# Kernel tuning notes

Measured on AMD Instinct MI355X. Metric: run time of the kernel, lower is better.

The kernel has to match this reference:

```python
import jax, jax.numpy as jnp
import numpy as np

D_MODEL, N_HEADS, N_KV_HEADS = 2048, 16, 4
D_HEAD = D_MODEL // N_HEADS  # 128
N_REP = N_HEADS // N_KV_HEADS  # 4
B, S = 2, 2048
ROPE_THETA = 10000.0


def setup_inputs() -> dict:
    key = jax.random.key(0)
    ks = jax.random.split(key, 6)
    x = jax.random.normal(ks[0], (B, S, D_MODEL), dtype=jnp.float32)
    # RoPE frequencies (real/imag parts of freqs_cis)
    inv_freq = 1.0 / (ROPE_THETA ** (np.arange(0, D_HEAD, 2, dtype=np.float32) / D_HEAD))
    angles = np.arange(S, dtype=np.float32)[:, None] * inv_freq[None, :]  # [S, D_HEAD//2]
    freqs_cos = jnp.asarray(np.cos(angles))
    freqs_sin = jnp.asarray(np.sin(angles))
    # causal additive mask [1,1,S,S]
    causal = jnp.tril(jnp.ones((S, S), dtype=bool))
    mask = jnp.where(causal, 0.0, -1e9).astype(jnp.float32)[None, None]
    scale = 0.02
    wq = jax.random.normal(ks[1], (D_MODEL, N_HEADS * D_HEAD), dtype=jnp.float32) * scale
    wk = jax.random.normal(ks[2], (D_MODEL, N_KV_HEADS * D_HEAD), dtype=jnp.float32) * scale
    wv = jax.random.normal(ks[3], (D_MODEL, N_KV_HEADS * D_HEAD), dtype=jnp.float32) * scale
    wo = jax.random.normal(ks[4], (N_HEADS * D_HEAD, D_MODEL), dtype=jnp.float32) * scale
    return {"x": x, "freqs_cos": freqs_cos, "freqs_sin": freqs_sin, "mask": mask,
            "wq": wq, "wk": wk, "wv": wv, "wo": wo}


def _apply_rope(t, cos, sin):
    # t: [B, S, H, D]; cos/sin: [S, D//2] -> complex rotation on interleaved pairs
    tr = t.reshape(*t.shape[:-1], -1, 2)
    xr, xi = tr[..., 0], tr[..., 1]
    c = cos[None, :, None, :]
    s = sin[None, :, None, :]
    out_r = xr * c - xi * s
    out_i = xr * s + xi * c
    return jnp.stack([out_r, out_i], axis=-1).reshape(t.shape)


def reference(x, freqs_cos, freqs_sin, mask, wq, wk, wv, wo):
    b, s, _ = x.shape
    xq = (x @ wq).reshape(b, s, N_HEADS, D_HEAD)
    xk = (x @ wk).reshape(b, s, N_KV_HEADS, D_HEAD)
    xv = (x @ wv).reshape(b, s, N_KV_HEADS, D_HEAD)
    xq = _apply_rope(xq, freqs_cos, freqs_sin)
    xk = _apply_rope(xk, freqs_cos, freqs_sin)
    # GQA: repeat each kv head n_rep times (head h uses kv head h // n_rep)
    xk = jnp.repeat(xk, N_REP, axis=2)  # [B,S,H,D]
    xv = jnp.repeat(xv, N_REP, axis=2)
    scores = jnp.einsum("bshd,bthd->bhst", xq, xk) / jnp.sqrt(jnp.float32(D_HEAD))
    scores = scores + mask
    probs = jax.nn.softmax(scores, axis=-1)
    out = jnp.einsum("bhst,bthd->bshd", probs, xv).reshape(b, s, N_HEADS * D_HEAD)
    return out @ wo
```

## Files before the change

kernel.cpp:

```cpp
#include <hip/hip_runtime.h>
#include <hip/hip_bf16.h>

#define BB 2
#define SS 2048
#define DM 2048
#define NH 16
#define NKV 4
#define DH 128
#define QS 3072

typedef __hip_bfloat16 bf16;
typedef short short8 __attribute__((ext_vector_type(8)));
typedef float floatx4 __attribute__((ext_vector_type(4)));

#if __has_builtin(__builtin_amdgcn_exp2f)
#define EX2(x) __builtin_amdgcn_exp2f(x)
#else
#define EX2(x) exp2f(x)
#endif

__device__ __forceinline__ bf16 f2b(float v) { return __float2bfloat16(v); }
__device__ __forceinline__ short f2bs(float v) {
    bf16 t = __float2bfloat16(v);
    return __builtin_bit_cast(short, t);
}
__device__ __forceinline__ void store_c(bf16* p, float v) { *p = __float2bfloat16(v); }
__device__ __forceinline__ void store_c(float* p, float v) { *p = v; }

__global__ __launch_bounds__(256) void convert_x(const float4* __restrict__ x,
                                                 bf16* __restrict__ xb, int n4) {
    int i = blockIdx.x * blockDim.x + threadIdx.x;
    if (i >= n4) return;
    float4 v = x[i];
    bf16* p = xb + (size_t)i * 4;
    p[0] = f2b(v.x); p[1] = f2b(v.y); p[2] = f2b(v.z); p[3] = f2b(v.w);
}

__global__ __launch_bounds__(256) void convert_wT(const float* __restrict__ w,
                                                  bf16* __restrict__ outT,
                                                  int N, int Kd) {
    const int n0 = blockIdx.x * 64, k0 = blockIdx.y * 64;
    __shared__ float tile[64][65];
    const int tid = threadIdx.x;
    for (int i = tid; i < 4096; i += 256) {
        int r = i >> 6, c = i & 63;
        tile[r][c] = w[(size_t)(k0 + r) * N + n0 + c];
    }
    __syncthreads();
    for (int i = tid; i < 4096; i += 256) {
        int r = i >> 6, c = i & 63;
        outT[(size_t)(n0 + r) * Kd + k0 + c] = f2b(tile[c][r]);
    }
}

template <typename TC>
__global__ __launch_bounds__(256) void mfma_gemm(const bf16* __restrict__ A,
                                                 const bf16* __restrict__ BT,
                                                 TC* __restrict__ C,
                                                 int M, int N, int K) {
    __shared__ short As[128 * 32];
    __shared__ short Bs[128 * 32];
    const int tid = threadIdx.x;
    const int w = tid >> 6, lane = tid & 63;
    const int col16 = lane & 15, quad = lane >> 4;
    const int row0 = blockIdx.y * 128, col0 = blockIdx.x * 128;
    const int wr0 = (w >> 1) * 64, wc0 = (w & 1) * 64;

    floatx4 acc[4][4];
    #pragma unroll
    for (int mi = 0; mi < 4; mi++)
        #pragma unroll
        for (int ni = 0; ni < 4; ni++) acc[mi][ni] = (floatx4){0.f, 0.f, 0.f, 0.f};

    for (int k0 = 0; k0 < K; k0 += 32) {
        __syncthreads();
        #pragma unroll
        for (int it = 0; it < 2; it++) {
            int c = w * 128 + it * 64 + lane;
            int r = c >> 2, seg = c & 3;
            const bf16* g = A + (size_t)(row0 + r) * K + k0 + seg * 8;
            __builtin_amdgcn_global_load_lds(
                (const __attribute__((address_space(1))) unsigned int*)g,
                (__attribute__((address_space(3))) unsigned int*)&As[(w * 128 + it * 64) * 8],
                16, 0, 0);
        }
        #pragma unroll
        for (int it = 0; it < 2; it++) {
            int c = w * 128 + it * 64 + lane;
            int r = c >> 2, seg = c & 3;
            const bf16* g = BT + (size_t)(col0 + r) * K + k0 + seg * 8;
            __builtin_amdgcn_global_load_lds(
                (const __attribute__((address_space(1))) unsigned int*)g,
                (__attribute__((address_space(3))) unsigned int*)&Bs[(w * 128 + it * 64) * 8],
                16, 0, 0);
        }
        __syncthreads();

        short8 af[4], bfr[4];
        #pragma unroll
        for (int mi = 0; mi < 4; mi++)
            af[mi] = *(const short8*)&As[(wr0 + mi * 16 + col16) * 32 + quad * 8];
        #pragma unroll
        for (int ni = 0; ni < 4; ni++)
            bfr[ni] = *(const short8*)&Bs[(wc0 + ni * 16 + col16) * 32 + quad * 8];
        #pragma unroll
        for (int mi = 0; mi < 4; mi++)
            #pragma unroll
            for (int ni = 0; ni < 4; ni++)
                acc[mi][ni] = __builtin_amdgcn_mfma_f32_16x16x32_bf16(af[mi], bfr[ni], acc[mi][ni], 0, 0, 0);
    }
    #pragma unroll
    for (int mi = 0; mi < 4; mi++)
        #pragma unroll
        for (int ni = 0; ni < 4; ni++)
            #pragma unroll
            for (int r = 0; r < 4; r++)
                store_c(&C[(size_t)(row0 + wr0 + mi * 16 + quad * 4 + r) * N +
                           col0 + wc0 + ni * 16 + col16],
                        acc[mi][ni][r]);
}

__global__ void rope_kernel(bf16* __restrict__ base, const float* __restrict__ cs,
                            const float* __restrict__ sn, int n_heads, int total) {
    int idx = blockIdx.x * blockDim.x + threadIdx.x;
    if (idx >= total) return;
    int i = idx & 63;
    int h = (idx >> 6) % n_heads;
    size_t bs = (size_t)idx / (64 * n_heads);
    int s = (int)(bs % SS);
    float c = cs[s * 64 + i];
    float si = sn[s * 64 + i];
    bf16* p = base + bs * QS + h * DH + 2 * i;
    float xr = __bfloat162float(p[0]), xi = __bfloat162float(p[1]);
    p[0] = f2b(xr * c - xi * si);
    p[1] = f2b(xr * si + xi * c);
}

__global__ __launch_bounds__(256) void transpose_v(const bf16* __restrict__ qkv,
                                                   bf16* __restrict__ vt) {
    const int s0 = blockIdx.x * 64, d0 = blockIdx.y * 64;
    const int b = blockIdx.z >> 2, kvh = blockIdx.z & 3;
    __shared__ bf16 tile[64][65];
    const int tid = threadIdx.x;
    for (int i = tid; i < 4096; i += 256) {
        int r = i >> 6, c = i & 63;
        tile[r][c] = qkv[(size_t)(b * SS + s0 + r) * QS + 2560 + kvh * DH + d0 + c];
    }
    __syncthreads();
    for (int i = tid; i < 4096; i += 256) {
        int r = i >> 6, c = i & 63;
        vt[((size_t)(b * NKV + kvh) * DH + d0 + r) * SS + s0 + c] = tile[c][r];
    }
}

#define PPAD 72

__global__ __launch_bounds__(256) void flash_attn(const bf16* __restrict__ qkv,
                                                  const bf16* __restrict__ vt,
                                                  bf16* __restrict__ ao) {
    const int bx = blockIdx.x, h = blockIdx.y, b = blockIdx.z;
    const int kvh = h >> 2;
    __shared__ short Ks[2][64 * 128];
    __shared__ short Vs[2][128 * 64];
    __shared__ short Ps[4 * 16 * PPAD];
    const int tid = threadIdx.x;
    const int w = tid >> 6, lane = tid & 63;
    const int col = lane & 15, quad = lane >> 4;
    const int c7 = col & 7;
    const float C = 0.12751746517859245f;

    const int krl = lane >> 4, kseg = lane & 15;
    const int vrl = lane >> 3, vseg = lane & 7;

    const bf16* kgb = qkv + (size_t)b * SS * QS + 2048 + kvh * DH;
    const bf16* vgb = vt + (size_t)(b * NKV + kvh) * DH * SS;

    const short8 vone = {0x3F80, 0x3F80, 0x3F80, 0x3F80, 0x3F80, 0x3F80, 0x3F80, 0x3F80};

    for (int phase = 0; phase < 2; phase++) {
        const int qt = phase == 0 ? bx : (SS / 64 - 1 - bx);
        const int q0 = qt * 64;

        short8 aq[4];
        const bf16* qbase = qkv + (size_t)(b * SS + q0 + w * 16 + col) * QS + h * DH;
        #pragma unroll
        for (int kc = 0; kc < 4; kc++)
            aq[kc] = *(const short8*)(qbase + kc * 32 + quad * 8);

        floatx4 o[8];
        #pragma unroll
        for (int dt = 0; dt < 8; dt++) o[dt] = (floatx4){0.f, 0.f, 0.f, 0.f};
        floatx4 oL = (floatx4){0.f, 0.f, 0.f, 0.f};
        float mrow[4] = {-3e38f, -3e38f, -3e38f, -3e38f};

        for (int kt = 0; kt <= qt; kt++) {
            const int cur = kt & 1;
            __syncthreads();
            if (kt == 0) {
                #pragma unroll
                for (int it = 0; it < 4; it++) {
                    int row = w * 16 + it * 4 + krl;
                    const bf16* g = kgb + (size_t)row * QS + ((kseg ^ (row & 7)) * 8);
                    __builtin_amdgcn_global_load_lds(
                        (const __attribute__((address_space(1))) unsigned int*)g,
                        (__attribute__((address_space(3))) unsigned int*)&Ks[0][(w * 16 + it * 4) * 128],
                        16, 0, 0);
                }
                #pragma unroll
                for (int it = 0; it < 4; it++) {
                    int drow = w * 32 + it * 8 + vrl;
                    const bf16* g = vgb + (size_t)drow * SS + ((vseg ^ (drow & 7)) * 8);
                    __builtin_amdgcn_global_load_lds(
                        (const __attribute__((address_space(1))) unsigned int*)g,
                        (__attribute__((address_space(3))) unsigned int*)&Vs[0][(w * 32 + it * 8) * 64],
                        16, 0, 0);
                }
                __syncthreads();
            }
            if (kt < qt) {
                const int nk0 = (kt + 1) * 64;
                #pragma unroll
                for (int it = 0; it < 4; it++) {
                    int row = w * 16 + it * 4 + krl;
                    const bf16* g = kgb + (size_t)(nk0 + row) * QS + ((kseg ^ (row & 7)) * 8);
                    __builtin_amdgcn_global_load_lds(
                        (const __attribute__((address_space(1))) unsigned int*)g,
                        (__attribute__((address_space(3))) unsigned int*)&Ks[cur ^ 1][(w * 16 + it * 4) * 128],
                        16, 0, 0);
                }
                #pragma unroll
                for (int it = 0; it < 4; it++) {
                    int drow = w * 32 + it * 8 + vrl;
                    const bf16* g = vgb + (size_t)drow * SS + nk0 + ((vseg ^ (drow & 7)) * 8);
                    __builtin_amdgcn_global_load_lds(
                        (const __attribute__((address_space(1))) unsigned int*)g,
                        (__attribute__((address_space(3))) unsigned int*)&Vs[cur ^ 1][(w * 32 + it * 8) * 64],
                        16, 0, 0);
                }
            }

            const int k0 = kt * 64;
            floatx4 s[4];
            __builtin_amdgcn_s_setprio(1);
            #pragma unroll
            for (int n = 0; n < 4; n++) {
                s[n] = (floatx4){0.f, 0.f, 0.f, 0.f};
                #pragma unroll
                for (int kc = 0; kc < 4; kc++) {
                    short8 bk = *(const short8*)&Ks[cur][(n * 16 + col) * 128 + (((kc * 4 + quad) ^ c7) * 8)];
                    s[n] = __builtin_amdgcn_mfma_f32_16x16x32_bf16(aq[kc], bk, s[n], 0, 0, 0);
                }
            }
            __builtin_amdgcn_s_setprio(0);

            if (kt == qt) {
                #pragma unroll
                for (int n = 0; n < 4; n++)
                    #pragma unroll
                    for (int r = 0; r < 4; r++)
                        if ((k0 + n * 16 + col) > (q0 + w * 16 + quad * 4 + r)) s[n][r] = -3e38f;
            }

            float rmx[4];
            #pragma unroll
            for (int r = 0; r < 4; r++) {
                float rm = fmaxf(fmaxf(s[0][r], s[1][r]), fmaxf(s[2][r], s[3][r]));
                rm = fmaxf(rm, __shfl_xor(rm, 1));
                rm = fmaxf(rm, __shfl_xor(rm, 2));
                rm = fmaxf(rm, __shfl_xor(rm, 4));
                rm = fmaxf(rm, __shfl_xor(rm, 8));
                rmx[r] = fmaxf(rm, mrow[r]);
            }
            bool grow = (rmx[0] > mrow[0]) | (rmx[1] > mrow[1]) |
                        (rmx[2] > mrow[2]) | (rmx[3] > mrow[3]);
            if (__any((int)grow)) {
                float al[4];
                #pragma unroll
                for (int r = 0; r < 4; r++) {
                    al[r] = EX2((mrow[r] - rmx[r]) * C);
                    mrow[r] = rmx[r];
                }
                #pragma unroll
                for (int dt = 0; dt < 8; dt++)
                    #pragma unroll
                    for (int r = 0; r < 4; r++) o[dt][r] *= al[r];
                #pragma unroll
                for (int r = 0; r < 4; r++) oL[r] *= al[r];
            }
            float mC[4];
            #pragma unroll
            for (int r = 0; r < 4; r++) mC[r] = mrow[r] * C;

            short* pw = &Ps[w * 16 * PPAD];
            #pragma unroll
            for (int n = 0; n < 4; n++)
                #pragma unroll
                for (int r = 0; r < 4; r++)
                    pw[(quad * 4 + r) * PPAD + n * 16 + col] =
                        f2bs(EX2(__builtin_fmaf(s[n][r], C, -mC[r])));

            short8 ap0 = *(const short8*)&pw[col * PPAD + quad * 8];
            short8 ap1 = *(const short8*)&pw[col * PPAD + 32 + quad * 8];
            __builtin_amdgcn_s_setprio(1);
            #pragma unroll
            for (int dt = 0; dt < 8; dt++) {
                short8 bv0 = *(const short8*)&Vs[cur][(dt * 16 + col) * 64 + ((quad ^ c7) * 8)];
                o[dt] = __builtin_amdgcn_mfma_f32_16x16x32_bf16(ap0, bv0, o[dt], 0, 0, 0);
                short8 bv1 = *(const short8*)&Vs[cur][(dt * 16 + col) * 64 + (((quad + 4) ^ c7) * 8)];
                o[dt] = __builtin_amdgcn_mfma_f32_16x16x32_bf16(ap1, bv1, o[dt], 0, 0, 0);
            }
            oL = __builtin_amdgcn_mfma_f32_16x16x32_bf16(ap0, vone, oL, 0, 0, 0);
            oL = __builtin_amdgcn_mfma_f32_16x16x32_bf16(ap1, vone, oL, 0, 0, 0);
            __builtin_amdgcn_s_setprio(0);
        }
        #pragma unroll
        for (int r = 0; r < 4; r++) {
            float inv = 1.f / oL[r];
            int srow = q0 + w * 16 + quad * 4 + r;
            bf16* op = ao + ((size_t)(b * SS + srow) * NH + h) * DH;
            #pragma unroll
            for (int dt = 0; dt < 8; dt++)
                op[dt * 16 + col] = f2b(o[dt][r] * inv);
        }
    }
}

extern "C" void kernel_launch(void* const* d_in, const int* in_sizes, int n_in,
                              void* d_out, int out_size, void* d_ws, size_t ws_size,
                              hipStream_t stream) {
    const float* x  = (const float*)d_in[0];
    const float* fc = (const float*)d_in[1];
    const float* fs = (const float*)d_in[2];
    const float* wq = (const float*)d_in[4];
    const float* wk = (const float*)d_in[5];
    const float* wv = (const float*)d_in[6];
    const float* wo = (const float*)d_in[7];
    float* out = (float*)d_out;

    const int M = BB * SS;
    bf16* qkv    = (bf16*)d_ws;
    bf16* xb     = qkv + (size_t)M * QS;
    bf16* wqkvT  = xb + (size_t)M * DM;
    bf16* ao     = xb;
    bf16* vt     = wqkvT;
    bf16* woT    = qkv;

    dim3 blk(256);
    convert_x<<<(M * DM / 4 + 255) / 256, blk, 0, stream>>>((const float4*)x, xb, M * DM / 4);
    convert_wT<<<dim3(DM / 64, DM / 64), blk, 0, stream>>>(wq, wqkvT, DM, DM);
    convert_wT<<<dim3((NKV * DH) / 64, DM / 64), blk, 0, stream>>>(wk, wqkvT + (size_t)2048 * DM, NKV * DH, DM);
    convert_wT<<<dim3((NKV * DH) / 64, DM / 64), blk, 0, stream>>>(wv, wqkvT + (size_t)2560 * DM, NKV * DH, DM);

    mfma_gemm<bf16><<<dim3(QS / 128, M / 128), blk, 0, stream>>>(xb, wqkvT, qkv, M, QS, DM);

    const int totq = BB * SS * NH * 64;
    const int totk = BB * SS * NKV * 64;
    rope_kernel<<<(totq + 255) / 256, blk, 0, stream>>>(qkv, fc, fs, NH, totq);
    rope_kernel<<<(totk + 255) / 256, blk, 0, stream>>>(qkv + 2048, fc, fs, NKV, totk);

    transpose_v<<<dim3(SS / 64, DH / 64, BB * NKV), blk, 0, stream>>>(qkv, vt);

    flash_attn<<<dim3(SS / 128, NH, BB), blk, 0, stream>>>(qkv, vt, ao);

    convert_wT<<<dim3(DM / 64, DM / 64), blk, 0, stream>>>(wo, woT, DM, DM);
    mfma_gemm<float><<<dim3(DM / 128, M / 128), blk, 0, stream>>>(ao, woT, out, M, DM, DM);
}
```

Baseline: 366.3 us.

## Triple-buffer GEMM LDS loads with swizzle and merge weight-convert and RoPE launches

The bf16 MFMA GEMM now uses a three-stage LDS ring with async global-to-LDS loads issued two tiles ahead, so each k-step needs one barrier instead of two. An XOR swizzle on the 16-byte segments reduces LDS bank conflicts on the fragment reads, and the MFMA block is wrapped in raised wave priority. Separately, the three q/k/v weight-transpose launches are merged into one kernel and the two RoPE launches into one, which cuts launch overhead. The GEMM now uses three times as much LDS, which may lower occupancy.

```diff
diff --git a/kernel.cpp b/kernel.cpp
--- a/kernel.cpp
+++ b/kernel.cpp
@@ -53,18 +53,67 @@
     }
 }
 
+__global__ __launch_bounds__(256) void convert_wqkv(const float* __restrict__ wq,
+                                                    const float* __restrict__ wk,
+                                                    const float* __restrict__ wv,
+                                                    bf16* __restrict__ outT) {
+    const int bx = blockIdx.x;
+    const float* w; int N; int n0;
+    if (bx < 32)      { w = wq; N = 2048; n0 = bx * 64; }
+    else if (bx < 40) { w = wk; N = 512;  n0 = (bx - 32) * 64; }
+    else              { w = wv; N = 512;  n0 = (bx - 40) * 64; }
+    const int k0 = blockIdx.y * 64;
+    const int gn0 = bx * 64;
+    __shared__ float tile[64][65];
+    const int tid = threadIdx.x;
+    for (int i = tid; i < 4096; i += 256) {
+        int r = i >> 6, c = i & 63;
+        tile[r][c] = w[(size_t)(k0 + r) * N + n0 + c];
+    }
+    __syncthreads();
+    for (int i = tid; i < 4096; i += 256) {
+        int r = i >> 6, c = i & 63;
+        outT[(size_t)(gn0 + r) * DM + k0 + c] = f2b(tile[c][r]);
+    }
+}
+
 template <typename TC>
 __global__ __launch_bounds__(256) void mfma_gemm(const bf16* __restrict__ A,
                                                  const bf16* __restrict__ BT,
                                                  TC* __restrict__ C,
                                                  int M, int N, int K) {
-    __shared__ short As[128 * 32];
-    __shared__ short Bs[128 * 32];
+    __shared__ short As[3][128 * 32];
+    __shared__ short Bs[3][128 * 32];
     const int tid = threadIdx.x;
     const int w = tid >> 6, lane = tid & 63;
     const int col16 = lane & 15, quad = lane >> 4;
     const int row0 = blockIdx.y * 128, col0 = blockIdx.x * 128;
     const int wr0 = (w >> 1) * 64, wc0 = (w & 1) * 64;
+    const int nt = K / 32;
+
+    auto issue = [&](int t, int b) {
+        const int k0 = t * 32;
+        #pragma unroll
+        for (int it = 0; it < 2; it++) {
+            int cc = w * 128 + it * 64 + lane;
+            int r = cc >> 2, seg = cc & 3;
+            const bf16* g = A + (size_t)(row0 + r) * K + k0 + ((seg ^ (r & 3)) * 8);
+            __builtin_amdgcn_global_load_lds(
+                (const __attribute__((address_space(1))) unsigned int*)g,
+                (__attribute__((address_space(3))) unsigned int*)&As[b][(w * 128 + it * 64) * 8],
+                16, 0, 0);
+        }
+        #pragma unroll
+        for (int it = 0; it < 2; it++) {
+            int cc = w * 128 + it * 64 + lane;
+            int r = cc >> 2, seg = cc & 3;
+            const bf16* g = BT + (size_t)(col0 + r) * K + k0 + ((seg ^ (r & 3)) * 8);
+            __builtin_amdgcn_global_load_lds(
+                (const __attribute__((address_space(1))) unsigned int*)g,
+                (__attribute__((address_space(3))) unsigned int*)&Bs[b][(w * 128 + it * 64) * 8],
+                16, 0, 0);
+        }
+    };
 
     floatx4 acc[4][4];
     #pragma unroll
@@ -72,42 +121,36 @@
         #pragma unroll
         for (int ni = 0; ni < 4; ni++) acc[mi][ni] = (floatx4){0.f, 0.f, 0.f, 0.f};
 
-    for (int k0 = 0; k0 < K; k0 += 32) {
-        __syncthreads();
-        #pragma unroll
-        for (int it = 0; it < 2; it++) {
-            int c = w * 128 + it * 64 + lane;
-            int r = c >> 2, seg = c & 3;
-            const bf16* g = A + (size_t)(row0 + r) * K + k0 + seg * 8;
-            __builtin_amdgcn_global_load_lds(
-                (const __attribute__((address_space(1))) unsigned int*)g,
-                (__attribute__((address_space(3))) unsigned int*)&As[(w * 128 + it * 64) * 8],
-                16, 0, 0);
-        }
-        #pragma unroll
-        for (int it = 0; it < 2; it++) {
-            int c = w * 128 + it * 64 + lane;
-            int r = c >> 2, seg = c & 3;
-            const bf16* g = BT + (size_t)(col0 + r) * K + k0 + seg * 8;
-            __builtin_amdgcn_global_load_lds(
-                (const __attribute__((address_space(1))) unsigned int*)g,
-                (__attribute__((address_space(3))) unsigned int*)&Bs[(w * 128 + it * 64) * 8],
-                16, 0, 0);
-        }
-        __syncthreads();
+    issue(0, 0);
+    if (1 < nt) issue(1, 1);
+
+    for (int t = 0; t < nt; ++t) {
+        const int cb = t % 3;
+        if (t + 1 < nt) { asm volatile("s_waitcnt vmcnt(4)" ::: "memory"); }
+        else            { asm volatile("s_waitcnt vmcnt(0)" ::: "memory"); }
+        __builtin_amdgcn_sched_barrier(0);
+        __builtin_amdgcn_s_barrier();
+        __builtin_amdgcn_sched_barrier(0);
+        if (t + 2 < nt) issue(t + 2, (t + 2) % 3);
 
         short8 af[4], bfr[4];
         #pragma unroll
-        for (int mi = 0; mi < 4; mi++)
-            af[mi] = *(const short8*)&As[(wr0 + mi * 16 + col16) * 32 + quad * 8];
-        #pragma unroll
-        for (int ni = 0; ni < 4; ni++)
-            bfr[ni] = *(const short8*)&Bs[(wc0 + ni * 16 + col16) * 32 + quad * 8];
+        for (int mi = 0; mi < 4; mi++) {
+            int r = wr0 + mi * 16 + col16;
+            af[mi] = *(const short8*)&As[cb][r * 32 + ((quad ^ (r & 3)) * 8)];
+        }
+        #pragma unroll
+        for (int ni = 0; ni < 4; ni++) {
+            int r = wc0 + ni * 16 + col16;
+            bfr[ni] = *(const short8*)&Bs[cb][r * 32 + ((quad ^ (r & 3)) * 8)];
+        }
+        __builtin_amdgcn_s_setprio(1);
         #pragma unroll
         for (int mi = 0; mi < 4; mi++)
             #pragma unroll
             for (int ni = 0; ni < 4; ni++)
                 acc[mi][ni] = __builtin_amdgcn_mfma_f32_16x16x32_bf16(af[mi], bfr[ni], acc[mi][ni], 0, 0, 0);
+        __builtin_amdgcn_s_setprio(0);
     }
     #pragma unroll
     for (int mi = 0; mi < 4; mi++)
@@ -120,13 +163,16 @@
                         acc[mi][ni][r]);
 }
 
-__global__ void rope_kernel(bf16* __restrict__ base, const float* __restrict__ cs,
-                            const float* __restrict__ sn, int n_heads, int total) {
+__global__ void rope_all(bf16* __restrict__ qkv, const float* __restrict__ cs,
+                         const float* __restrict__ sn, int totq, int total) {
     int idx = blockIdx.x * blockDim.x + threadIdx.x;
     if (idx >= total) return;
-    int i = idx & 63;
-    int h = (idx >> 6) % n_heads;
-    size_t bs = (size_t)idx / (64 * n_heads);
+    bf16* base; int n_heads; int rel;
+    if (idx < totq) { base = qkv;        n_heads = NH;  rel = idx; }
+    else            { base = qkv + 2048; n_heads = NKV; rel = idx - totq; }
+    int i = rel & 63;
+    int h = (rel >> 6) % n_heads;
+    size_t bs = (size_t)rel / (64 * n_heads);
     int s = (int)(bs % SS);
     float c = cs[s * 64 + i];
     float si = sn[s * 64 + i];
@@ -347,16 +393,13 @@
 
     dim3 blk(256);
     convert_x<<<(M * DM / 4 + 255) / 256, blk, 0, stream>>>((const float4*)x, xb, M * DM / 4);
-    convert_wT<<<dim3(DM / 64, DM / 64), blk, 0, stream>>>(wq, wqkvT, DM, DM);
-    convert_wT<<<dim3((NKV * DH) / 64, DM / 64), blk, 0, stream>>>(wk, wqkvT + (size_t)2048 * DM, NKV * DH, DM);
-    convert_wT<<<dim3((NKV * DH) / 64, DM / 64), blk, 0, stream>>>(wv, wqkvT + (size_t)2560 * DM, NKV * DH, DM);
+    convert_wqkv<<<dim3(QS / 64, DM / 64), blk, 0, stream>>>(wq, wk, wv, wqkvT);
 
     mfma_gemm<bf16><<<dim3(QS / 128, M / 128), blk, 0, stream>>>(xb, wqkvT, qkv, M, QS, DM);
 
     const int totq = BB * SS * NH * 64;
     const int totk = BB * SS * NKV * 64;
-    rope_kernel<<<(totq + 255) / 256, blk, 0, stream>>>(qkv, fc, fs, NH, totq);
-    rope_kernel<<<(totk + 255) / 256, blk, 0, stream>>>(qkv + 2048, fc, fs, NKV, totk);
+    rope_all<<<(totq + totk + 255) / 256, blk, 0, stream>>>(qkv, fc, fs, totq, totq + totk);
 
     transpose_v<<<dim3(SS / 64, DH / 64, BB * NKV), blk, 0, stream>>>(qkv, vt);
 
```

After: 345.5 us. -5.7%, faster.
